# Performance work log

Measured on AMD Instinct MI355X. Metric: run time of the kernel, lower is better.

## Reference

```python
import jax, jax.numpy as jnp
import numpy as np
import math

# batch, seq_len, emb_ch, convlru_hidden_ch, spatial H, W (W must equal H, see diag_embed broadcast)
B, L, E, C, H, W = 4, 32, 64, 96, 32, 32


def setup_inputs():
    key = jax.random.key(0)
    ks = jax.random.split(key, 24)
    r_min, r_max = 0.8, 0.99
    u1 = jax.random.uniform(ks[0], (C, H))
    u2 = jax.random.uniform(ks[1], (C, H))
    nu_log = jnp.log(-0.5 * jnp.log(u1 * (r_max ** 2 - r_min ** 2) + r_min ** 2))
    theta_log = jnp.log(u2 * 2.0 * np.pi)
    lam_abs = jnp.exp(-jnp.exp(nu_log))  # |lambda| = exp(-nu)
    gamma_log = jnp.log(jnp.sqrt(1.0 - lam_abs ** 2))
    params_log = jnp.vstack([nu_log, theta_log, gamma_log]).astype(jnp.float32)

    def w(k, shape, fan_in):
        s = 1.0 / np.sqrt(fan_in)
        return jax.random.uniform(k, shape, minval=-s, maxval=s, dtype=jnp.float32)

    return {
        "x": jax.random.normal(ks[2], (B, L, E, H, W), jnp.float32),
        "mask": jnp.ones((B, L), jnp.float32),
        "params_log": params_log,
        "Wb_r": w(ks[3], (C, E), E), "Wb_i": w(ks[4], (C, E), E),
        "bb_r": w(ks[5], (C,), E), "bb_i": w(ks[6], (C,), E),
        "Wp1_r": w(ks[7], (C, C), C), "Wp1_i": w(ks[8], (C, C), C),
        "bp1_r": w(ks[9], (C,), C), "bp1_i": w(ks[10], (C,), C),
        "Wp2_r": w(ks[11], (C, C), C), "Wp2_i": w(ks[12], (C, C), C),
        "bp2_r": w(ks[13], (C,), C), "bp2_i": w(ks[14], (C,), C),
        "Wc_r": w(ks[15], (E, C), C), "Wc_i": w(ks[16], (E, C), C),
        "bc_r": w(ks[17], (E,), C), "bc_i": w(ks[18], (E,), C),
        "ln_w": jnp.ones((E, H, W), jnp.float32),
        "ln_b": jnp.zeros((E, H, W), jnp.float32),
    }


def _forward(x, mask, params_log, Wb, bb, Wp1, bp1, Wp2, bp2, Wc, bc, ln_w, ln_b):
    nu, theta, gamma = jnp.split(jnp.exp(params_log), 3, axis=0)  # each (C, H)
    lamb = jnp.exp(jnp.complex64(-nu + 1j * theta))               # (C, H)
    xc = x.astype(jnp.complex64)
    # proj_B: 1x1 complex conv == channel einsum
    h = jnp.einsum('blehw,ce->blchw', xc, Wb) + bb[:, None, None]
    h = jnp.fft.fft2(h)  # over last two axes
    h = jnp.einsum('blkhw,ck->blchw', h, Wp1) + bp1[:, None, None]
    eye = jnp.eye(H, dtype=jnp.float32)  # (H, W); requires W == H
    # h * torch.diag_embed(gamma): elementwise mult with a diagonal (C,H,H) matrix
    # -> zeroes off-diagonal spatial entries (faithful to the torch code)
    h = h * (gamma[:, :, None] * eye)
    m = jnp.broadcast_to(mask[:, :, None, None, None], h.shape).astype(jnp.float32)
    log2L = int(math.ceil(math.log2(L)))
    lamb = lamb[None]  # (1, C, H)
    for i in range(1, log2L + 1):
        l = 2 ** i
        if i > 1:
            lamb = jnp.concatenate([lamb, lamb * lamb[-1]], axis=0)  # (l//2, C, H)
        hr = h.reshape(B * L // l, l, C, H, W)
        mr = m.reshape(B * L // l, l, C, H, W)
        h1, h2 = hr[:, : l // 2], hr[:, l // 2:]
        # term[n,j,c,a,b] = lamb[j,c,a] * eye[a,b] * h1[n,-1,c,a,b] * mask[n,l//2-1,c,a,b]
        term = (lamb[None, :, :, :, None] * eye) * h1[:, -1:] * mr[:, l // 2 - 1: l // 2]
        h = jnp.concatenate([h1, h2 + term], axis=1).reshape(B, L, C, H, W)
    h = jnp.fft.ifft2(h)
    h = jnp.einsum('blkhw,ck->blchw', h, Wp2) + bp2[:, None, None]
    h = jnp.einsum('blchw,ec->blehw', h, Wc) + bc[:, None, None]
    h = h.real
    # dropout is identity in eval mode
    mu = jnp.mean(h, axis=(-3, -2, -1), keepdims=True)
    var = jnp.var(h, axis=(-3, -2, -1), keepdims=True)
    h = (h - mu) / jnp.sqrt(var + 1e-5) * ln_w + ln_b
    return h + x


def reference(x, mask, params_log, Wb_r, Wb_i, bb_r, bb_i, Wp1_r, Wp1_i, bp1_r, bp1_i, Wp2_r, Wp2_i, bp2_r, bp2_i, Wc_r, Wc_i, bc_r, bc_i, ln_w, ln_b):
    cx = lambda r, i: (r + 1j * i).astype(jnp.complex64)
    return _forward(x, mask, params_log,
                    cx(Wb_r, Wb_i), cx(bb_r, bb_i),
                    cx(Wp1_r, Wp1_i), cx(bp1_r, bp1_i),
                    cx(Wp2_r, Wp2_i), cx(bp2_r, bp2_i),
                    cx(Wc_r, Wc_i), cx(bc_r, bc_i),
                    ln_w, ln_b)
```

## Files before the change

### kernel.cpp

```cpp
#include <hip/hip_runtime.h>

static constexpr int BL = 128;
static constexpr int OFF_COS  = 0;
static constexpr int OFF_SIN  = 1024;
static constexpr int OFF_ARE  = 2048;
static constexpr int OFF_AIM  = 8192;
static constexpr int OFF_WRE  = 14336;
static constexpr int OFF_WIM  = 20480;
static constexpr int OFF_LRE  = 26624;
static constexpr int OFF_LIM  = 29696;
static constexpr int OFF_GAM  = 32768;
static constexpr int OFF_BH0R = 35840;
static constexpr int OFF_BH0I = 35936;
static constexpr int OFF_BRR  = 36032;
static constexpr int OFF_QF   = 36096;
static constexpr int OFF_Y    = 560384;
static constexpr int OFF_R    = 1871104;
static constexpr int OFF_ST   = 2133248;

__global__ __launch_bounds__(256) void kA(
    const float* __restrict__ x,
    const float* __restrict__ params_log,
    const float* __restrict__ Wb_r, const float* __restrict__ Wb_i,
    const float* __restrict__ bb_r, const float* __restrict__ bb_i,
    const float* __restrict__ Wp1_r, const float* __restrict__ Wp1_i,
    const float* __restrict__ Wp2_r, const float* __restrict__ Wp2_i,
    const float* __restrict__ Wc_r, const float* __restrict__ Wc_i,
    const float* __restrict__ bp2_r, const float* __restrict__ bp2_i,
    const float* __restrict__ bc_r, float* __restrict__ ws) {
  if (blockIdx.x < 2048) {
    __shared__ float pl[4][1024];
    __shared__ float qsh[4][32];
    __shared__ float ct[32], st[32];
    int wave = threadIdx.x >> 6, lane = threadIdx.x & 63;
    if (threadIdx.x < 32) {
      float sv, cv;
      sincosf((float)threadIdx.x * 0.19634954084936207f, &sv, &cv);
      ct[threadIdx.x] = cv;
      st[threadIdx.x] = sv;
    }
    int plane = blockIdx.x * 4 + wave;
    const float4* xp = (const float4*)(x + (size_t)plane * 1024);
    float4* pl4 = (float4*)pl[wave];
#pragma unroll
    for (int j = 0; j < 4; ++j) pl4[j * 64 + lane] = xp[j * 64 + lane];
    __syncthreads();
    int s = lane & 31, halfw = lane >> 5;
    float acc = 0.f;
#pragma unroll
    for (int u0 = 0; u0 < 16; ++u0) {
      int u = halfw * 16 + u0;
      acc += pl[wave][u * 32 + ((s - u) & 31)];
    }
    acc += __shfl_xor(acc, 32);
    if (lane < 32) qsh[wave][lane] = acc;
    __syncthreads();
    int h = lane & 31;
    const float* T = (lane < 32) ? ct : st;
    float sum = 0.f;
    int m = 0;
#pragma unroll
    for (int s2 = 0; s2 < 32; ++s2) {
      sum += qsh[wave][s2] * T[m];
      m = (m + h) & 31;
    }
    if (lane >= 32) sum = -sum;
    ws[OFF_QF + (size_t)plane * 64 + h * 2 + (lane < 32 ? 0 : 1)] = sum;
  } else {
    int tid = (int)(blockIdx.x - 2048) * 256 + threadIdx.x;
    if (tid < 3072) {
      int i = tid;
      float nu = expf(params_log[i]);
      float th = expf(params_log[3072 + i]);
      float g  = expf(params_log[6144 + i]);
      float rr = expf(-nu);
      ws[OFF_LRE + i] = rr * cosf(th);
      ws[OFF_LIM + i] = rr * sinf(th);
      ws[OFF_GAM + i] = g;
    } else if (tid < 9216) {
      int i = tid - 3072;
      int c = i >> 6, e = i & 63;
      float are = 0.f, aim = 0.f;
      for (int k = 0; k < 96; ++k) {
        float pr = Wp1_r[c * 96 + k], pi = Wp1_i[c * 96 + k];
        float wr = Wb_r[k * 64 + e], wi = Wb_i[k * 64 + e];
        are += pr * wr - pi * wi;
        aim += pr * wi + pi * wr;
      }
      ws[OFF_ARE + i] = are;
      ws[OFF_AIM + i] = aim;
    } else if (tid < 15360) {
      int i = tid - 9216;
      int e = i / 96, c = i - e * 96;
      float are = 0.f, aim = 0.f;
      for (int k = 0; k < 96; ++k) {
        float wr = Wc_r[e * 96 + k], wi = Wc_i[e * 96 + k];
        float pr = Wp2_r[k * 96 + c], pi = Wp2_i[k * 96 + c];
        are += wr * pr - wi * pi;
        aim += wr * pi + wi * pr;
      }
      ws[OFF_WRE + i] = are;
      ws[OFF_WIM + i] = aim;
    } else if (tid < 15456) {
      int c = tid - 15360;
      float re = 0.f, im = 0.f;
      for (int k = 0; k < 96; ++k) {
        float pr = Wp1_r[c * 96 + k], pi = Wp1_i[c * 96 + k];
        float br = bb_r[k], bi = bb_i[k];
        re += pr * br - pi * bi;
        im += pr * bi + pi * br;
      }
      ws[OFF_BH0R + c] = 1024.f * re;
      ws[OFF_BH0I + c] = 1024.f * im;
    } else if (tid < 15520) {
      int e = tid - 15456;
      float re = 0.f;
      for (int k = 0; k < 96; ++k)
        re += Wc_r[e * 96 + k] * bp2_r[k] - Wc_i[e * 96 + k] * bp2_i[k];
      ws[OFF_BRR + e] = re + bc_r[e];
    }
  }
}

__global__ __launch_bounds__(256) void kB(float* __restrict__ ws,
                                          const float* __restrict__ bp1_r,
                                          const float* __restrict__ bp1_i) {
  __shared__ float2 q[64][32];
  int bl = blockIdx.x / 12, chunk = blockIdx.x % 12;
  const float2* qF = (const float2*)(ws + OFF_QF) + bl * 2048;
  for (int i = threadIdx.x; i < 2048; i += 256) q[i >> 5][i & 31] = qF[i];
  __syncthreads();
  int c = chunk * 8 + (threadIdx.x >> 5), h = threadIdx.x & 31;
  const float* Ar = ws + OFF_ARE + c * 64;
  const float* Ai = ws + OFF_AIM + c * 64;
  float re = 0.f, im = 0.f;
#pragma unroll 8
  for (int e = 0; e < 64; ++e) {
    float ar = Ar[e], ai = Ai[e];
    float2 qv = q[e][h];
    re += ar * qv.x - ai * qv.y;
    im += ar * qv.y + ai * qv.x;
  }
  if (h == 0) { re += ws[OFF_BH0R + c]; im += ws[OFF_BH0I + c]; }
  re += bp1_r[c];
  im += bp1_i[c];
  float g = ws[OFF_GAM + c * 32 + h];
  ((float2*)(ws + OFF_Y))[(bl * 96 + c) * 32 + h] = make_float2(g * re, g * im);
}

__global__ __launch_bounds__(64) void kC(float* __restrict__ ws,
                                         const float* __restrict__ mask) {
  int tid = blockIdx.x * 64 + threadIdx.x;
  int b = tid / 3072, r = tid - b * 3072;
  float lr = ws[OFF_LRE + r], li = ws[OFF_LIM + r];
  float2* Y = (float2*)(ws + OFF_Y) + (size_t)b * 3072 * 32 + r;
  float2 v[32];
#pragma unroll
  for (int l = 0; l < 32; ++l) v[l] = Y[(size_t)l * 3072];
  float sr = v[0].x, si = v[0].y;
#pragma unroll
  for (int l = 1; l < 32; ++l) {
    float mk = mask[b * 32 + l - 1];
    float cr = mk * (lr * sr - li * si);
    float ci = mk * (lr * si + li * sr);
    sr = v[l].x + cr;
    si = v[l].y + ci;
    v[l] = make_float2(sr, si);
  }
#pragma unroll
  for (int l = 1; l < 32; ++l) Y[(size_t)l * 3072] = v[l];
}

__global__ __launch_bounds__(256) void kD(float* __restrict__ ws) {
  __shared__ float2 S[96][32];
  __shared__ float2 V[32][33];
  __shared__ float ct[32], st[32];
  __shared__ float red[8];
  int bl = blockIdx.x >> 1, half = blockIdx.x & 1;
  const float2* Sg = (const float2*)(ws + OFF_Y) + bl * 3072;
  for (int i = threadIdx.x; i < 3072; i += 256) S[i >> 5][i & 31] = Sg[i];
  if (threadIdx.x < 32) {
    float sv, cv;
    sincosf((float)threadIdx.x * 0.19634954084936207f, &sv, &cv);
    ct[threadIdx.x] = cv;
    st[threadIdx.x] = sv;
  }
  __syncthreads();
  int h = threadIdx.x & 31, g = threadIdx.x >> 5;
  float vr[4] = {0.f, 0.f, 0.f, 0.f}, vi[4] = {0.f, 0.f, 0.f, 0.f};
  int ebase = half * 32 + g;
#pragma unroll 4
  for (int c = 0; c < 96; ++c) {
    float2 s = S[c][h];
#pragma unroll
    for (int k = 0; k < 4; ++k) {
      int e = ebase + k * 8;
      float wr = ws[OFF_WRE + e * 96 + c];
      float wi = ws[OFF_WIM + e * 96 + c];
      vr[k] += wr * s.x - wi * s.y;
      vi[k] += wr * s.y + wi * s.x;
    }
  }
#pragma unroll
  for (int k = 0; k < 4; ++k) V[k * 8 + g][h] = make_float2(vr[k], vi[k]);
  __syncthreads();
  float* R = ws + OFF_R + bl * 2048 + half * 1024;
  float sum = 0.f, sumsq = 0.f;
#pragma unroll
  for (int k = 0; k < 4; ++k) {
    int idx = k * 256 + threadIdx.x;
    int el = idx >> 5, s2 = idx & 31;
    float acc = 0.f;
    int m = 0;
#pragma unroll
    for (int hh = 0; hh < 32; ++hh) {
      float2 v = V[el][hh];
      acc += v.x * ct[m] - v.y * st[m];
      m = (m + s2) & 31;
    }
    float r = acc * (1.0f / 1024.0f) + ws[OFF_BRR + half * 32 + el];
    R[idx] = r;
    sum += r;
    sumsq += r * r;
  }
#pragma unroll
  for (int off = 32; off > 0; off >>= 1) {
    sum += __shfl_down(sum, off);
    sumsq += __shfl_down(sumsq, off);
  }
  int wave = threadIdx.x >> 6, lane = threadIdx.x & 63;
  if (lane == 0) { red[wave] = sum; red[4 + wave] = sumsq; }
  __syncthreads();
  if (threadIdx.x == 0) {
    ws[OFF_ST + bl * 4 + half * 2]     = red[0] + red[1] + red[2] + red[3];
    ws[OFF_ST + bl * 4 + half * 2 + 1] = red[4] + red[5] + red[6] + red[7];
  }
}

__global__ __launch_bounds__(256) void kE(const float* __restrict__ x,
                                          const float* __restrict__ lnw,
                                          const float* __restrict__ lnb,
                                          const float* __restrict__ ws,
                                          float* __restrict__ out) {
  __shared__ float Rs[32];
  int bl = blockIdx.x >> 6, e = blockIdx.x & 63;
  if (threadIdx.x < 32)
    Rs[threadIdx.x] = ws[OFF_R + bl * 2048 + e * 32 + threadIdx.x];
  const float* stp = ws + OFF_ST + bl * 4;
  float s0 = stp[0] + stp[2], q0 = stp[1] + stp[3];
  float mu = s0 * (1.0f / 2048.0f);
  float istd = rsqrtf(q0 * (1.0f / 2048.0f) - mu * mu + 1e-5f);
  __syncthreads();
  int gid = blockIdx.x * 256 + threadIdx.x;
  int pos = threadIdx.x * 4;
  int u = pos >> 5, v = pos & 31;
  int rem4 = e * 256 + threadIdx.x;
  const float4 xin = ((const float4*)x)[gid];
  const float4 lw = ((const float4*)lnw)[rem4];
  const float4 lb = ((const float4*)lnb)[rem4];
  float4 o;
  o.x = (Rs[(u + v) & 31] - mu) * istd * lw.x + lb.x + xin.x;
  o.y = (Rs[(u + v + 1) & 31] - mu) * istd * lw.y + lb.y + xin.y;
  o.z = (Rs[(u + v + 2) & 31] - mu) * istd * lw.z + lb.z + xin.z;
  o.w = (Rs[(u + v + 3) & 31] - mu) * istd * lw.w + lb.w + xin.w;
  ((float4*)out)[gid] = o;
}

extern "C" void kernel_launch(void* const* d_in, const int* in_sizes, int n_in,
                              void* d_out, int out_size, void* d_ws, size_t ws_size,
                              hipStream_t stream) {
  const float* x          = (const float*)d_in[0];
  const float* mask       = (const float*)d_in[1];
  const float* params_log = (const float*)d_in[2];
  const float* Wb_r  = (const float*)d_in[3];
  const float* Wb_i  = (const float*)d_in[4];
  const float* bb_r  = (const float*)d_in[5];
  const float* bb_i  = (const float*)d_in[6];
  const float* Wp1_r = (const float*)d_in[7];
  const float* Wp1_i = (const float*)d_in[8];
  const float* bp1_r = (const float*)d_in[9];
  const float* bp1_i = (const float*)d_in[10];
  const float* Wp2_r = (const float*)d_in[11];
  const float* Wp2_i = (const float*)d_in[12];
  const float* bp2_r = (const float*)d_in[13];
  const float* bp2_i = (const float*)d_in[14];
  const float* Wc_r  = (const float*)d_in[15];
  const float* Wc_i  = (const float*)d_in[16];
  const float* bc_r  = (const float*)d_in[17];
  const float* ln_w  = (const float*)d_in[19];
  const float* ln_b  = (const float*)d_in[20];
  float* ws  = (float*)d_ws;
  float* out = (float*)d_out;

  kA<<<2109, 256, 0, stream>>>(x, params_log, Wb_r, Wb_i, bb_r, bb_i,
                               Wp1_r, Wp1_i, Wp2_r, Wp2_i, Wc_r, Wc_i,
                               bp2_r, bp2_i, bc_r, ws);
  kB<<<1536, 256, 0, stream>>>(ws, bp1_r, bp1_i);
  kC<<<192, 64, 0, stream>>>(ws, mask);
  kD<<<256, 256, 0, stream>>>(ws);
  kE<<<8192, 256, 0, stream>>>(x, ln_w, ln_b, ws, out);
}
```

Measured before the change: 170.7 us.

## Fuse projection with recurrence scan and output projection with layernorm epilogue

The four post-FFT kernels become two. kBC computes the Wp1 projection for one (batch, h) slice into shared memory and then runs the sequential lambda recurrence over L in the same block. kDE has each block compute all 64 output channels, recomputing the work of its sibling block, so the layernorm statistics stay in shared memory and the normalized residual output is written directly. This removes two launches and the global round trips of the intermediate R and statistics buffers. The cost is duplicated Wc and inverse-DFT compute, and a streaming epilogue that runs on only 256 blocks, which may use less memory bandwidth than the old 8192-block kernel.

Measured after the change: 193.4 us. 1.13x slower.

```diff
diff --git a/kernel.cpp b/kernel.cpp
--- a/kernel.cpp
+++ b/kernel.cpp
@@ -1,8 +1,6 @@
 #include <hip/hip_runtime.h>
 
 static constexpr int BL = 128;
-static constexpr int OFF_COS  = 0;
-static constexpr int OFF_SIN  = 1024;
 static constexpr int OFF_ARE  = 2048;
 static constexpr int OFF_AIM  = 8192;
 static constexpr int OFF_WRE  = 14336;
@@ -15,8 +13,6 @@
 static constexpr int OFF_BRR  = 36032;
 static constexpr int OFF_QF   = 36096;
 static constexpr int OFF_Y    = 560384;
-static constexpr int OFF_R    = 1871104;
-static constexpr int OFF_ST   = 2133248;
 
 __global__ __launch_bounds__(256) void kA(
     const float* __restrict__ x,
@@ -122,62 +118,82 @@
   }
 }
 
-__global__ __launch_bounds__(256) void kB(float* __restrict__ ws,
-                                          const float* __restrict__ bp1_r,
-                                          const float* __restrict__ bp1_i) {
-  __shared__ float2 q[64][32];
-  int bl = blockIdx.x / 12, chunk = blockIdx.x % 12;
-  const float2* qF = (const float2*)(ws + OFF_QF) + bl * 2048;
-  for (int i = threadIdx.x; i < 2048; i += 256) q[i >> 5][i & 31] = qF[i];
-  __syncthreads();
-  int c = chunk * 8 + (threadIdx.x >> 5), h = threadIdx.x & 31;
-  const float* Ar = ws + OFF_ARE + c * 64;
-  const float* Ai = ws + OFF_AIM + c * 64;
-  float re = 0.f, im = 0.f;
+__global__ __launch_bounds__(256) void kBC(float* __restrict__ ws,
+                                           const float* __restrict__ mask,
+                                           const float* __restrict__ bp1_r,
+                                           const float* __restrict__ bp1_i) {
+  __shared__ float qre[32][65], qim[32][65];
+  __shared__ float Yre[48][33], Yim[48][33];
+  __shared__ float msh[32];
+  int b = blockIdx.x >> 6;
+  int h = (blockIdx.x >> 1) & 31;
+  int ch = blockIdx.x & 1;
+  const float2* qF2 = (const float2*)(ws + OFF_QF);
+  for (int i = threadIdx.x; i < 2048; i += 256) {
+    int l = i >> 6, e = i & 63;
+    float2 v = qF2[(size_t)(b * 2048 + l * 64 + e) * 32 + h];
+    qre[l][e] = v.x;
+    qim[l][e] = v.y;
+  }
+  if (threadIdx.x < 32) msh[threadIdx.x] = mask[b * 32 + threadIdx.x];
+  __syncthreads();
+  int l = threadIdx.x & 31, cg = threadIdx.x >> 5;
+  int cbase = ch * 48 + cg * 6;
+  float yr[6] = {0.f, 0.f, 0.f, 0.f, 0.f, 0.f};
+  float yi[6] = {0.f, 0.f, 0.f, 0.f, 0.f, 0.f};
 #pragma unroll 8
   for (int e = 0; e < 64; ++e) {
-    float ar = Ar[e], ai = Ai[e];
-    float2 qv = q[e][h];
-    re += ar * qv.x - ai * qv.y;
-    im += ar * qv.y + ai * qv.x;
-  }
-  if (h == 0) { re += ws[OFF_BH0R + c]; im += ws[OFF_BH0I + c]; }
-  re += bp1_r[c];
-  im += bp1_i[c];
-  float g = ws[OFF_GAM + c * 32 + h];
-  ((float2*)(ws + OFF_Y))[(bl * 96 + c) * 32 + h] = make_float2(g * re, g * im);
+    float qr = qre[l][e], qi_ = qim[l][e];
+#pragma unroll
+    for (int k = 0; k < 6; ++k) {
+      int c = cbase + k;
+      float ar = ws[OFF_ARE + c * 64 + e];
+      float ai = ws[OFF_AIM + c * 64 + e];
+      yr[k] += ar * qr - ai * qi_;
+      yi[k] += ar * qi_ + ai * qr;
+    }
+  }
+#pragma unroll
+  for (int k = 0; k < 6; ++k) {
+    int c = cbase + k;
+    float re = yr[k] + bp1_r[c];
+    float im = yi[k] + bp1_i[c];
+    if (h == 0) { re += ws[OFF_BH0R + c]; im += ws[OFF_BH0I + c]; }
+    float g = ws[OFF_GAM + c * 32 + h];
+    Yre[cg * 6 + k][l] = g * re;
+    Yim[cg * 6 + k][l] = g * im;
+  }
+  __syncthreads();
+  if (threadIdx.x < 48) {
+    int cl = threadIdx.x, c = ch * 48 + cl;
+    float lr = ws[OFF_LRE + c * 32 + h], li = ws[OFF_LIM + c * 32 + h];
+    float2* Sg = (float2*)(ws + OFF_Y);
+    float sr = Yre[cl][0], si = Yim[cl][0];
+    Sg[((size_t)(b * 32 + 0) * 96 + c) * 32 + h] = make_float2(sr, si);
+    for (int l2 = 1; l2 < 32; ++l2) {
+      float mk = msh[l2 - 1];
+      float cr = mk * (lr * sr - li * si);
+      float ci = mk * (lr * si + li * sr);
+      sr = Yre[cl][l2] + cr;
+      si = Yim[cl][l2] + ci;
+      Sg[((size_t)(b * 32 + l2) * 96 + c) * 32 + h] = make_float2(sr, si);
+    }
+  }
 }
 
-__global__ __launch_bounds__(64) void kC(float* __restrict__ ws,
-                                         const float* __restrict__ mask) {
-  int tid = blockIdx.x * 64 + threadIdx.x;
-  int b = tid / 3072, r = tid - b * 3072;
-  float lr = ws[OFF_LRE + r], li = ws[OFF_LIM + r];
-  float2* Y = (float2*)(ws + OFF_Y) + (size_t)b * 3072 * 32 + r;
-  float2 v[32];
-#pragma unroll
-  for (int l = 0; l < 32; ++l) v[l] = Y[(size_t)l * 3072];
-  float sr = v[0].x, si = v[0].y;
-#pragma unroll
-  for (int l = 1; l < 32; ++l) {
-    float mk = mask[b * 32 + l - 1];
-    float cr = mk * (lr * sr - li * si);
-    float ci = mk * (lr * si + li * sr);
-    sr = v[l].x + cr;
-    si = v[l].y + ci;
-    v[l] = make_float2(sr, si);
-  }
-#pragma unroll
-  for (int l = 1; l < 32; ++l) Y[(size_t)l * 3072] = v[l];
-}
-
-__global__ __launch_bounds__(256) void kD(float* __restrict__ ws) {
-  __shared__ float2 S[96][32];
-  __shared__ float2 V[32][33];
+__global__ __launch_bounds__(256) void kDE(const float* __restrict__ x,
+                                           const float* __restrict__ lnw,
+                                           const float* __restrict__ lnb,
+                                           float* __restrict__ ws,
+                                           float* __restrict__ out) {
+  __shared__ float2 S[96][33];
+  __shared__ float2 V[64][33];
+  __shared__ float Rsh[64][32];
   __shared__ float ct[32], st[32];
   __shared__ float red[8];
+  __shared__ float stats[2];
   int bl = blockIdx.x >> 1, half = blockIdx.x & 1;
-  const float2* Sg = (const float2*)(ws + OFF_Y) + bl * 3072;
+  const float2* Sg = (const float2*)(ws + OFF_Y) + (size_t)bl * 3072;
   for (int i = threadIdx.x; i < 3072; i += 256) S[i >> 5][i & 31] = Sg[i];
   if (threadIdx.x < 32) {
     float sv, cv;
@@ -187,14 +203,14 @@
   }
   __syncthreads();
   int h = threadIdx.x & 31, g = threadIdx.x >> 5;
-  float vr[4] = {0.f, 0.f, 0.f, 0.f}, vi[4] = {0.f, 0.f, 0.f, 0.f};
-  int ebase = half * 32 + g;
+  float vr[8] = {0.f, 0.f, 0.f, 0.f, 0.f, 0.f, 0.f, 0.f};
+  float vi[8] = {0.f, 0.f, 0.f, 0.f, 0.f, 0.f, 0.f, 0.f};
 #pragma unroll 4
   for (int c = 0; c < 96; ++c) {
     float2 s = S[c][h];
 #pragma unroll
-    for (int k = 0; k < 4; ++k) {
-      int e = ebase + k * 8;
+    for (int k = 0; k < 8; ++k) {
+      int e = g + k * 8;
       float wr = ws[OFF_WRE + e * 96 + c];
       float wi = ws[OFF_WIM + e * 96 + c];
       vr[k] += wr * s.x - wi * s.y;
@@ -202,14 +218,13 @@
     }
   }
 #pragma unroll
-  for (int k = 0; k < 4; ++k) V[k * 8 + g][h] = make_float2(vr[k], vi[k]);
-  __syncthreads();
-  float* R = ws + OFF_R + bl * 2048 + half * 1024;
+  for (int k = 0; k < 8; ++k) V[g + k * 8][h] = make_float2(vr[k], vi[k]);
+  __syncthreads();
   float sum = 0.f, sumsq = 0.f;
-#pragma unroll
-  for (int k = 0; k < 4; ++k) {
-    int idx = k * 256 + threadIdx.x;
-    int el = idx >> 5, s2 = idx & 31;
+  int s2 = threadIdx.x & 31;
+#pragma unroll
+  for (int k = 0; k < 8; ++k) {
+    int el = k * 8 + (threadIdx.x >> 5);
     float acc = 0.f;
     int m = 0;
 #pragma unroll
@@ -218,8 +233,8 @@
       acc += v.x * ct[m] - v.y * st[m];
       m = (m + s2) & 31;
     }
-    float r = acc * (1.0f / 1024.0f) + ws[OFF_BRR + half * 32 + el];
-    R[idx] = r;
+    float r = acc * (1.0f / 1024.0f) + ws[OFF_BRR + el];
+    Rsh[el][s2] = r;
     sum += r;
     sumsq += r * r;
   }
@@ -232,38 +247,35 @@
   if (lane == 0) { red[wave] = sum; red[4 + wave] = sumsq; }
   __syncthreads();
   if (threadIdx.x == 0) {
-    ws[OFF_ST + bl * 4 + half * 2]     = red[0] + red[1] + red[2] + red[3];
-    ws[OFF_ST + bl * 4 + half * 2 + 1] = red[4] + red[5] + red[6] + red[7];
-  }
-}
-
-__global__ __launch_bounds__(256) void kE(const float* __restrict__ x,
-                                          const float* __restrict__ lnw,
-                                          const float* __restrict__ lnb,
-                                          const float* __restrict__ ws,
-                                          float* __restrict__ out) {
-  __shared__ float Rs[32];
-  int bl = blockIdx.x >> 6, e = blockIdx.x & 63;
-  if (threadIdx.x < 32)
-    Rs[threadIdx.x] = ws[OFF_R + bl * 2048 + e * 32 + threadIdx.x];
-  const float* stp = ws + OFF_ST + bl * 4;
-  float s0 = stp[0] + stp[2], q0 = stp[1] + stp[3];
-  float mu = s0 * (1.0f / 2048.0f);
-  float istd = rsqrtf(q0 * (1.0f / 2048.0f) - mu * mu + 1e-5f);
-  __syncthreads();
-  int gid = blockIdx.x * 256 + threadIdx.x;
-  int pos = threadIdx.x * 4;
-  int u = pos >> 5, v = pos & 31;
-  int rem4 = e * 256 + threadIdx.x;
-  const float4 xin = ((const float4*)x)[gid];
-  const float4 lw = ((const float4*)lnw)[rem4];
-  const float4 lb = ((const float4*)lnb)[rem4];
-  float4 o;
-  o.x = (Rs[(u + v) & 31] - mu) * istd * lw.x + lb.x + xin.x;
-  o.y = (Rs[(u + v + 1) & 31] - mu) * istd * lw.y + lb.y + xin.y;
-  o.z = (Rs[(u + v + 2) & 31] - mu) * istd * lw.z + lb.z + xin.z;
-  o.w = (Rs[(u + v + 3) & 31] - mu) * istd * lw.w + lb.w + xin.w;
-  ((float4*)out)[gid] = o;
+    float s0 = red[0] + red[1] + red[2] + red[3];
+    float q0 = red[4] + red[5] + red[6] + red[7];
+    float mu = s0 * (1.0f / 2048.0f);
+    stats[0] = mu;
+    stats[1] = rsqrtf(q0 * (1.0f / 2048.0f) - mu * mu + 1e-5f);
+  }
+  __syncthreads();
+  float mu = stats[0], istd = stats[1];
+  const float4* x4 = (const float4*)x;
+  const float4* lw4 = (const float4*)lnw;
+  const float4* lb4 = (const float4*)lnb;
+  float4* o4 = (float4*)out;
+  int t = threadIdx.x;
+  int u = t >> 3, v0 = (t & 7) * 4;
+#pragma unroll 4
+  for (int it = 0; it < 32; ++it) {
+    int e = half * 32 + it;
+    int gid = bl * 16384 + e * 256 + t;
+    int rem = e * 256 + t;
+    float4 xin = x4[gid];
+    float4 lw = lw4[rem];
+    float4 lb = lb4[rem];
+    float4 o;
+    o.x = (Rsh[e][(u + v0) & 31] - mu) * istd * lw.x + lb.x + xin.x;
+    o.y = (Rsh[e][(u + v0 + 1) & 31] - mu) * istd * lw.y + lb.y + xin.y;
+    o.z = (Rsh[e][(u + v0 + 2) & 31] - mu) * istd * lw.z + lb.z + xin.z;
+    o.w = (Rsh[e][(u + v0 + 3) & 31] - mu) * istd * lw.w + lb.w + xin.w;
+    o4[gid] = o;
+  }
 }
 
 extern "C" void kernel_launch(void* const* d_in, const int* in_sizes, int n_in,
@@ -295,8 +307,6 @@
   kA<<<2109, 256, 0, stream>>>(x, params_log, Wb_r, Wb_i, bb_r, bb_i,
                                Wp1_r, Wp1_i, Wp2_r, Wp2_i, Wc_r, Wc_i,
                                bp2_r, bp2_i, bc_r, ws);
-  kB<<<1536, 256, 0, stream>>>(ws, bp1_r, bp1_i);
-  kC<<<192, 64, 0, stream>>>(ws, mask);
-  kD<<<256, 256, 0, stream>>>(ws);
-  kE<<<8192, 256, 0, stream>>>(x, ln_w, ln_b, ws, out);
+  kBC<<<256, 256, 0, stream>>>(ws, mask, bp1_r, bp1_i);
+  kDE<<<256, 256, 0, stream>>>(x, ln_w, ln_b, ws, out);
 }
```
